# Optimization experiments

Hardware: AMD Instinct MI355X
Metric: run time of the kernel (lower is better)

Reference implementation:

```python
import jax, jax.numpy as jnp
import numpy as np

D = 512       # hidden_size (attention defaults hardcode 512)
N = 8         # num_heads
H = D // N    # depth per head = 64
FF = 2048     # FFN filter size (hardcoded)
EPS = 1e-6


def _layer_norm(x, gamma, beta):
    # matches functional layer_norm: biased variance, eps inside sqrt
    mean = jnp.mean(x, axis=-1, keepdims=True)
    var = jnp.mean((x - mean) ** 2, axis=-1, keepdims=True)
    return gamma * ((x - mean) / jnp.sqrt(var + EPS)) + beta


def setup_inputs() -> dict:
    key = jax.random.key(0)
    ks = jax.random.split(key, 12)
    B, S = 8, 1024
    s = lambda k, shape, scale: jax.random.normal(k, shape, jnp.float32) * scale
    return {
        "inputs": s(ks[0], (B, S, D), 1.0),
        "attention_bias": jnp.zeros((B, 1, 1, S), jnp.float32),
        "ln1_g": jnp.ones((D,), jnp.float32),
        "ln1_b": jnp.zeros((D,), jnp.float32),
        "wq": s(ks[1], (D, N, H), D ** -0.5),
        "wk": s(ks[2], (D, N, H), D ** -0.5),
        "wv": s(ks[3], (D, N, H), D ** -0.5),
        "wo": s(ks[4], (N, H, D), D ** -0.5),
        "ln2_g": jnp.ones((D,), jnp.float32),
        "ln2_b": jnp.zeros((D,), jnp.float32),
        "w1": s(ks[5], (D, FF), D ** -0.5),
        "b1": jnp.zeros((FF,), jnp.float32),
        "w2": s(ks[6], (FF, D), FF ** -0.5),
        "b2": jnp.zeros((D,), jnp.float32),
    }


def reference(inputs, attention_bias, ln1_g, ln1_b, wq, wk, wv, wo,
              ln2_g, ln2_b, w1, b1, w2, b2):
    # --- self-attention block (pre-LN, residual) ---
    y = _layer_norm(inputs, ln1_g, ln1_b)
    q = jnp.einsum('bsd,dnh->bsnh', y, wq) * (H ** -0.5)
    k = jnp.einsum('bsd,dnh->bsnh', y, wk)
    v = jnp.einsum('bsd,dnh->bsnh', y, wv)
    # logits[b,n,f,t] = sum_h k[b,t,n,h] * q[b,f,n,h]
    logits = jnp.einsum('btnh,bfnh->bnft', k, q) + attention_bias
    weights = jax.nn.softmax(logits, axis=3)
    attn = jnp.einsum('bnft,btnh->bfnh', weights, v)
    attn_out = jnp.einsum('bfnh,nhd->bfd', attn, wo)
    x = inputs + attn_out

    # --- FFN block (pre-LN, residual) ---
    y2 = _layer_norm(x, ln2_g, ln2_b)
    h = jax.nn.relu(jnp.einsum('bsd,df->bsf', y2, w1) + b1)
    ffn_out = jnp.einsum('bsf,fd->bsd', h, w2) + b2
    return x + ffn_out
```

## Files before the change

### kernel.cpp

```cpp
#include <hip/hip_runtime.h>
#include <stdint.h>

typedef unsigned short u16;
typedef __attribute__((ext_vector_type(8))) __bf16 bf16x8;
typedef __attribute__((ext_vector_type(2))) __bf16 bf16x2;
typedef __attribute__((ext_vector_type(4))) float f32x4;

__device__ __forceinline__ float bf2f(u16 u) {
    union { unsigned int i; float f; } c; c.i = ((unsigned int)u) << 16; return c.f;
}
__device__ __forceinline__ u16 f2bf_sw(float f) {
    union { float f; unsigned int i; } c; c.f = f;
    unsigned int u = c.i;
    u += 0x7FFFu + ((u >> 16) & 1u);
    return (u16)(u >> 16);
}
__device__ __forceinline__ unsigned f2bf2(float lo, float hi) {
#if __has_builtin(__builtin_amdgcn_cvt_pk_bf16_f32)
    union { bf16x2 v; unsigned u; } c;
    c.v = __builtin_amdgcn_cvt_pk_bf16_f32(lo, hi);
    return c.u;
#else
    return (unsigned)f2bf_sw(lo) | ((unsigned)f2bf_sw(hi) << 16);
#endif
}
__device__ __forceinline__ u16 f2bf(float f) {
#if __has_builtin(__builtin_amdgcn_cvt_pk_bf16_f32)
    return (u16)(f2bf2(f, 0.f) & 0xFFFFu);
#else
    return f2bf_sw(f);
#endif
}
__device__ __forceinline__ bool sniff_f32(const unsigned* probe) {
    return probe && ((*probe & 0xFFFFu) == 0u);
}
__device__ __forceinline__ float lde(const void* p, size_t i, bool isf32) {
    return isf32 ? ((const float*)p)[i] : bf2f(((const u16*)p)[i]);
}
__device__ __forceinline__ void g2lds16(const void* g, void* l) {
    __builtin_amdgcn_global_load_lds(
        (__attribute__((address_space(1))) void*)(uintptr_t)g,
        (__attribute__((address_space(3))) void*)(unsigned int)(uintptr_t)l,
        16, 0, 0);
}
__device__ __forceinline__ void fence_bar() {
    __builtin_amdgcn_sched_barrier(0);
    __builtin_amdgcn_s_barrier();
    __builtin_amdgcn_sched_barrier(0);
}

__global__ void prep_weights(const void* __restrict__ wq, const void* __restrict__ wk,
                             const void* __restrict__ wv, const void* __restrict__ wo,
                             const void* __restrict__ w1, const void* __restrict__ w2,
                             u16* __restrict__ wqkvT, u16* __restrict__ woT,
                             u16* __restrict__ w1T, u16* __restrict__ w2T,
                             const unsigned* probe) {
    __shared__ u16 t[32][33];
    const bool isf32 = sniff_f32(probe);
    const int id = blockIdx.x;
    const void* src; u16* dst; int R, C, cb, rb; float scale = 1.f;
    if (id < 1024) {
        const int which = id >> 8, tl = id & 255;
        R = 512; C = 512; cb = (tl & 15) * 32; rb = (tl >> 4) * 32;
        if (which == 0)      { src = wq; dst = wqkvT;              scale = 0.18033688011112042f; }
        else if (which == 1) { src = wk; dst = wqkvT + 512 * 512; }
        else if (which == 2) { src = wv; dst = wqkvT + 1024 * 512; }
        else                 { src = wo; dst = woT; }
    } else if (id < 2048) {
        const int tl = id - 1024; src = w1; dst = w1T; R = 512; C = 2048;
        cb = (tl & 63) * 32; rb = (tl >> 6) * 32;
    } else {
        const int tl = id - 2048; src = w2; dst = w2T; R = 2048; C = 512;
        cb = (tl & 15) * 32; rb = (tl >> 4) * 32;
    }
    const int tx = threadIdx.x, ty = threadIdx.y;
#pragma unroll
    for (int i = 0; i < 4; i++)
        t[ty + i * 8][tx] = f2bf(lde(src, (size_t)(rb + ty + i * 8) * C + cb + tx, isf32));
    __syncthreads();
#pragma unroll
    for (int i = 0; i < 4; i++) {
        float v = bf2f(t[tx][ty + i * 8]) * scale;
        dst[(size_t)(cb + ty + i * 8) * R + rb + tx] = f2bf(v);
    }
}

__global__ __launch_bounds__(256) void ln_any(const void* __restrict__ x,
                                              const void* __restrict__ gw,
                                              const void* __restrict__ bw,
                                              u16* __restrict__ y,
                                              const unsigned* probe_x,
                                              const unsigned* probe_gb) {
    const bool xf32 = sniff_f32(probe_x);
    const bool gf32 = sniff_f32(probe_gb);
    const int lane = threadIdx.x & 63, wave = threadIdx.x >> 6;
    const int r = blockIdx.x * 4 + wave;
    union U8 { uint4 v; u16 s[8]; };
    float xs[8];
    if (xf32) {
        const float4* xr = (const float4*)((const float*)x + (size_t)r * 512 + lane * 8);
        float4 p0 = xr[0], p1 = xr[1];
        xs[0]=p0.x; xs[1]=p0.y; xs[2]=p0.z; xs[3]=p0.w;
        xs[4]=p1.x; xs[5]=p1.y; xs[6]=p1.z; xs[7]=p1.w;
    } else {
        U8 xu; xu.v = *(const uint4*)((const u16*)x + (size_t)r * 512 + lane * 8);
#pragma unroll
        for (int j = 0; j < 8; j++) xs[j] = bf2f(xu.s[j]);
    }
    float s1 = 0.f, s2 = 0.f;
#pragma unroll
    for (int j = 0; j < 8; j++) { s1 += xs[j]; s2 += xs[j] * xs[j]; }
#pragma unroll
    for (int d = 1; d < 64; d <<= 1) { s1 += __shfl_xor(s1, d); s2 += __shfl_xor(s2, d); }
    const float mean = s1 * (1.f / 512.f);
    const float var = s2 * (1.f / 512.f) - mean * mean;
    const float rstd = rsqrtf(var + 1e-6f);
    float gs[8], bs[8];
    if (gf32) {
        const float4* gr = (const float4*)((const float*)gw + lane * 8);
        const float4* br = (const float4*)((const float*)bw + lane * 8);
        float4 g0 = gr[0], g1 = gr[1], b0 = br[0], b1 = br[1];
        gs[0]=g0.x; gs[1]=g0.y; gs[2]=g0.z; gs[3]=g0.w; gs[4]=g1.x; gs[5]=g1.y; gs[6]=g1.z; gs[7]=g1.w;
        bs[0]=b0.x; bs[1]=b0.y; bs[2]=b0.z; bs[3]=b0.w; bs[4]=b1.x; bs[5]=b1.y; bs[6]=b1.z; bs[7]=b1.w;
    } else {
        U8 gu; gu.v = *(const uint4*)((const u16*)gw + lane * 8);
        U8 bu; bu.v = *(const uint4*)((const u16*)bw + lane * 8);
#pragma unroll
        for (int j = 0; j < 8; j++) { gs[j] = bf2f(gu.s[j]); bs[j] = bf2f(bu.s[j]); }
    }
    uint4 ov;
    float o[8];
#pragma unroll
    for (int j = 0; j < 8; j++) o[j] = gs[j] * ((xs[j] - mean) * rstd) + bs[j];
    ov.x = f2bf2(o[0], o[1]); ov.y = f2bf2(o[2], o[3]);
    ov.z = f2bf2(o[4], o[5]); ov.w = f2bf2(o[6], o[7]);
    *(uint4*)(y + (size_t)r * 512 + lane * 8) = ov;
}

template <int EPI, int TM>
__global__ __launch_bounds__(256, 2) void gemm_bt(const u16* __restrict__ A,
                                                  const u16* __restrict__ Bt,
                                                  const void* __restrict__ bias,
                                                  const void* __restrict__ res,
                                                  void* __restrict__ out,
                                                  u16* __restrict__ out2,
                                                  const unsigned* probe,
                                                  int M, int N, int K) {
    constexpr int ACH = TM / 16;
    constexpr int MI = TM / 32;
    __shared__ __align__(16) u16 lA[2][TM * 32];
    __shared__ __align__(16) u16 lB[2][128 * 32];
    const int tid = threadIdx.x, wave = tid >> 6, lane = tid & 63;
    const int m0 = blockIdx.x * TM, n0 = blockIdx.y * 128;
    const int wm = (wave >> 1) * (TM / 2), wn = (wave & 1) * 64;
    const int row = lane & 15, quad = lane >> 4;
    f32x4 acc[MI][4];
#pragma unroll
    for (int i = 0; i < MI; i++)
#pragma unroll
        for (int j = 0; j < 4; j++) acc[i][j] = (f32x4){0.f, 0.f, 0.f, 0.f};
    const u16* Ab = A + (size_t)m0 * K;
    const u16* Bb = Bt + (size_t)n0 * K;

    auto stage = [&](int buf, int k0) {
#pragma unroll
        for (int c = 0; c < (ACH + 8 + 3) / 4; c++) {
            const int ch = c * 4 + wave;
            if (ch < ACH) {
                const int e = ch * 64 + lane;
                const int r = e >> 2, col = (e & 3) * 8;
                g2lds16(Ab + (size_t)r * K + k0 + col, (char*)lA[buf] + ch * 1024);
            } else if (ch < ACH + 8) {
                const int c2 = ch - ACH;
                const int e = c2 * 64 + lane;
                const int r = e >> 2, col = (e & 3) * 8;
                g2lds16(Bb + (size_t)r * K + k0 + col, (char*)lB[buf] + c2 * 1024);
            }
        }
    };

    stage(0, 0);
    int cur = 0;
    for (int k0 = 0; k0 < K; k0 += 32) {
        __syncthreads();
        if (k0 + 32 < K) stage(cur ^ 1, k0 + 32);
        bf16x8 af[MI], bfr[4];
#pragma unroll
        for (int t = 0; t < MI; t++)
            af[t]  = *(const bf16x8*)(lA[cur] + (wm + t * 16 + row) * 32 + quad * 8);
#pragma unroll
        for (int t = 0; t < 4; t++)
            bfr[t] = *(const bf16x8*)(lB[cur] + (wn + t * 16 + row) * 32 + quad * 8);
#pragma unroll
        for (int i = 0; i < MI; i++)
#pragma unroll
            for (int j = 0; j < 4; j++)
                acc[i][j] = __builtin_amdgcn_mfma_f32_16x16x32_bf16(af[i], bfr[j], acc[i][j], 0, 0, 0);
        cur ^= 1;
    }
    const bool isf32 = sniff_f32(probe);
#pragma unroll
    for (int i = 0; i < MI; i++) {
        const int gm = m0 + wm + i * 16 + quad * 4;
#pragma unroll
        for (int j = 0; j < 4; j++) {
            const int gn = n0 + wn + j * 16 + row;
            float bv = 0.f;
            if (EPI == 2 || EPI == 3) bv = lde(bias, gn, isf32);
#pragma unroll
            for (int r = 0; r < 4; r++) {
                float v = acc[i][j][r];
                const int gmr = gm + r;
                size_t idx = (size_t)gmr * N + gn;
                if (EPI == 1) {
                    ((u16*)out)[idx] = f2bf(v + lde(res, idx, isf32));
                } else if (EPI == 2) {
                    v += bv;
                    ((u16*)out)[idx] = f2bf(v > 0.f ? v : 0.f);
                } else if (EPI == 3) {
                    v += bv + bf2f(((const u16*)res)[idx]);
                    if (isf32) ((float*)out)[idx] = v;
                    else       ((u16*)out)[idx] = f2bf(v);
                } else {
                    if (gn < 1024) {
                        ((u16*)out)[(size_t)gmr * 1024 + gn] = f2bf(v);
                    } else {
                        const int j2 = gn - 1024, n = j2 >> 6, h2 = j2 & 63;
                        const int b = gmr >> 10, t = gmr & 1023;
                        const int ut = t & 31, vt = ut & 15;
                        const int tP = (t & ~31) | ((vt >> 2) * 8 + ((ut >> 4) << 2) + (vt & 3));
                        out2[(((size_t)b * 8 + n) * 64 + h2) * 1024 + tP] = f2bf(v);
                    }
                }
            }
        }
    }
}

__global__ __launch_bounds__(512, 8) void attn_fused(const u16* __restrict__ qk,
                                                     const u16* __restrict__ vT,
                                                     const void* __restrict__ biasp,
                                                     u16* __restrict__ attn,
                                                     const unsigned* probe) {
    __shared__ __align__(16) char smem[36864];
    u16* lKb = (u16*)smem;
    u16* lVb = (u16*)(smem + 16384);
    char* lB = smem + 32768;
    const bool isf32 = sniff_f32(probe);
    const int tid = threadIdx.x, wave = tid >> 6, lane = tid & 63;
    const int wid = wave & 3, grp = wave >> 2;
    const int row = lane & 15, quad = lane >> 4;
    const int g0 = (quad ^ (row & 7)) * 8;
    const int gV = (quad ^ (row & 3)) * 8;
    const int bn = blockIdx.x, b = bn >> 3, n = bn & 7;
    const int f0 = blockIdx.y * 64;
    const u16* Qg = qk + (size_t)(b * 1024 + f0) * 1024 + n * 64;
    const u16* Kg = qk + (size_t)(b * 1024) * 1024 + 512 + n * 64;
    const u16* Vg = vT + (size_t)bn * 65536;

    auto stageKV = [&](int slot, int t0) {
        const int rk = wid * 8 + (lane >> 3);
        const int ck = ((lane & 7) ^ (rk & 7)) * 8;
        g2lds16(Kg + (size_t)(t0 + rk) * 1024 + ck, (char*)(lKb + slot * 2048) + wid * 1024);
        const int rv = wid * 16 + (lane >> 2);
        const int cv = ((lane & 3) ^ (rv & 3)) * 8;
        g2lds16(Vg + (size_t)rv * 1024 + t0 + cv, (char*)(lVb + slot * 2048) + wid * 1024);
    };

    bf16x8 bq[2];
    {
        const u16* qrow = Qg + (size_t)(wid * 16 + row) * 1024;
        bq[0] = *(const bf16x8*)(qrow + quad * 8);
        bq[1] = *(const bf16x8*)(qrow + (4 + quad) * 8);
    }
    if (grp == 0) {
        if (isf32)
            g2lds16((const float*)biasp + (size_t)b * 1024 + wid * 256 + lane * 4, lB + wid * 1024);
        else if (wid < 2)
            g2lds16((const u16*)biasp + (size_t)b * 1024 + wid * 512 + lane * 8, lB + wid * 1024);
    }
    stageKV(grp * 2,     grp * 32);
    stageKV(grp * 2 + 1, (2 + grp) * 32);
    asm volatile("s_waitcnt vmcnt(0)" ::: "memory");
    fence_bar();

    float l_i = 0.f;
    f32x4 oacc[4];
#pragma unroll
    for (int h = 0; h < 4; h++) oacc[h] = (f32x4){0.f, 0.f, 0.f, 0.f};

    auto compute = [&](int slot, int t0) {
        const u16* lKc = lKb + slot * 2048;
        const u16* lVc = lVb + slot * 2048;
        f32x4 s2[2];
        s2[0] = (f32x4){0.f, 0.f, 0.f, 0.f};
        s2[1] = (f32x4){0.f, 0.f, 0.f, 0.f};
#pragma unroll
        for (int nt = 0; nt < 2; nt++) {
            const int tr = nt * 16 + row;
            bf16x8 ak0 = *(const bf16x8*)(lKc + tr * 64 + g0);
            s2[nt] = __builtin_amdgcn_mfma_f32_16x16x32_bf16(ak0, bq[0], s2[nt], 0, 0, 0);
            bf16x8 ak1 = *(const bf16x8*)(lKc + tr * 64 + (g0 ^ 32));
            s2[nt] = __builtin_amdgcn_mfma_f32_16x16x32_bf16(ak1, bq[1], s2[nt], 0, 0, 0);
        }
#pragma unroll
        for (int nt = 0; nt < 2; nt++) {
            const int tl = t0 + nt * 16 + quad * 4;
            float bv4[4];
            if (isf32) {
                float4 t4 = *(const float4*)((const float*)lB + tl);
                bv4[0] = t4.x; bv4[1] = t4.y; bv4[2] = t4.z; bv4[3] = t4.w;
            } else {
                union { uint2 v; u16 s[4]; } bu;
                bu.v = *(const uint2*)((const u16*)lB + tl);
#pragma unroll
                for (int r = 0; r < 4; r++) bv4[r] = bf2f(bu.s[r]);
            }
#pragma unroll
            for (int r = 0; r < 4; r++) {
                float p = __builtin_exp2f(fmaf(bv4[r], 1.4426950408889634f, s2[nt][r]));
                s2[nt][r] = p;
                l_i += p;
            }
        }
        union { unsigned u[4]; bf16x8 v8; } bb;
        bb.u[0] = f2bf2(s2[0][0], s2[0][1]);
        bb.u[1] = f2bf2(s2[0][2], s2[0][3]);
        bb.u[2] = f2bf2(s2[1][0], s2[1][1]);
        bb.u[3] = f2bf2(s2[1][2], s2[1][3]);
#pragma unroll
        for (int ht = 0; ht < 4; ht++) {
            bf16x8 av = *(const bf16x8*)(lVc + (ht * 16 + row) * 32 + gV);
            oacc[ht] = __builtin_amdgcn_mfma_f32_16x16x32_bf16(av, bb.v8, oacc[ht], 0, 0, 0);
        }
    };

#pragma unroll 1
    for (int s = 0; s < 15; s++) {
        compute(grp * 2 + (s & 1), (2 * s + grp) * 32);
        fence_bar();
        if (s <= 13) {
            stageKV(grp * 2 + (s & 1), (2 * (s + 2) + grp) * 32);
            asm volatile("s_waitcnt vmcnt(2)" ::: "memory");
        } else {
            asm volatile("s_waitcnt vmcnt(0)" ::: "memory");
        }
        fence_bar();
    }
    compute(grp * 2 + 1, (30 + grp) * 32);

    __syncthreads();
    float* scr = (float*)smem;
    float* scrL = scr + 4608;
    if (grp == 1) {
#pragma unroll
        for (int ht = 0; ht < 4; ht++)
            *(f32x4*)(scr + wid * 1152 + (ht * 64 + lane) * 4) = oacc[ht];
        scrL[wid * 64 + lane] = l_i;
    }
    __syncthreads();
    if (grp == 0) {
#pragma unroll
        for (int ht = 0; ht < 4; ht++)
            oacc[ht] += *(const f32x4*)(scr + wid * 1152 + (ht * 64 + lane) * 4);
        l_i += scrL[wid * 64 + lane];
        l_i += __shfl_xor(l_i, 16);
        l_i += __shfl_xor(l_i, 32);
        const float inv = 1.f / l_i;
        const int f = f0 + wid * 16 + row;
#pragma unroll
        for (int ht = 0; ht < 4; ht++) {
            uint2 ov;
            ov.x = f2bf2(oacc[ht][0] * inv, oacc[ht][1] * inv);
            ov.y = f2bf2(oacc[ht][2] * inv, oacc[ht][3] * inv);
            *(uint2*)(attn + (size_t)(b * 1024 + f) * 512 + n * 64 + ht * 16 + quad * 4) = ov;
        }
    }
}

extern "C" void kernel_launch(void* const* d_in, const int* in_sizes, int n_in,
                              void* d_out, int out_size, void* d_ws, size_t ws_size,
                              hipStream_t stream) {
    const void* inp  = d_in[0];
    const void* ab   = d_in[1];
    const void* ln1g = d_in[2];
    const void* ln1b = d_in[3];
    const void* wq   = d_in[4];
    const void* wk   = d_in[5];
    const void* wv   = d_in[6];
    const void* wo   = d_in[7];
    const void* ln2g = d_in[8];
    const void* ln2b = d_in[9];
    const void* w1   = d_in[10];
    const void* b1   = d_in[11];
    const void* w2   = d_in[12];
    const void* b2   = d_in[13];
    const unsigned* probe = (const unsigned*)d_in[2];

    char* ws = (char*)d_ws;
    size_t off = 0;
    auto alloc = [&](size_t bytes) -> void* { void* p = ws + off; off += bytes; return p; };
    u16* wqkvT = (u16*)alloc(1536 * 512 * 2);
    u16* woT   = (u16*)alloc(512 * 512 * 2);
    u16* w1T   = (u16*)alloc(2048 * 512 * 2);
    u16* w2T   = (u16*)alloc(512 * 2048 * 2);
    u16* ybuf  = (u16*)alloc((size_t)8192 * 512 * 2);
    u16* qk    = (u16*)alloc((size_t)8192 * 1024 * 2);
    u16* vT    = (u16*)alloc((size_t)64 * 64 * 1024 * 2);
    u16* attn  = (u16*)alloc((size_t)8192 * 512 * 2);
    u16* xbf   = (u16*)alloc((size_t)8192 * 512 * 2);
    u16* hbuf  = qk;

    prep_weights<<<3072, dim3(32, 8), 0, stream>>>(wq, wk, wv, wo, w1, w2,
                                                   wqkvT, woT, w1T, w2T, probe);
    ln_any<<<2048, 256, 0, stream>>>(inp, ln1g, ln1b, ybuf, probe, probe);
    gemm_bt<4, 128><<<dim3(64, 12), 256, 0, stream>>>(ybuf, wqkvT, nullptr, nullptr, qk, vT, nullptr, 8192, 1536, 512);
    attn_fused<<<dim3(64, 16), 512, 0, stream>>>(qk, vT, ab, attn, probe);
    gemm_bt<1, 64><<<dim3(128, 4), 256, 0, stream>>>(attn, woT, nullptr, inp, xbf, nullptr, probe, 8192, 512, 512);
    ln_any<<<2048, 256, 0, stream>>>(xbf, ln2g, ln2b, ybuf, nullptr, probe);
    gemm_bt<2, 128><<<dim3(64, 16), 256, 0, stream>>>(ybuf, w1T, b1, nullptr, hbuf, nullptr, probe, 8192, 2048, 512);
    gemm_bt<3, 64><<<dim3(128, 4), 256, 0, stream>>>(hbuf, w2T, b2, xbf, (u16*)d_out, nullptr, probe, 8192, 512, 2048);
}
```

Measured before the change: 251.2 us.

## Fuse weight prep with LN1 and fuse Wo projection with residual and LN2

Merges the weight transpose kernel and the first layer norm into one launch using block-index ranges. Replaces the Wo GEMM plus the separate LN2 kernel with a new full-row GEMM (16 rows by 512 cols per block) that adds the residual, computes row mean and variance through shuffles and LDS partials, and writes both x and the normalized y. This removes two launches and an extra read of x. In exchange the new GEMM uses small M tiles, so each block re-streams the full Wo matrix and gets less reuse per block.

```diff
diff --git a/kernel.cpp b/kernel.cpp
--- a/kernel.cpp
+++ b/kernel.cpp
@@ -49,92 +49,88 @@
     __builtin_amdgcn_sched_barrier(0);
 }
 
-__global__ void prep_weights(const void* __restrict__ wq, const void* __restrict__ wk,
-                             const void* __restrict__ wv, const void* __restrict__ wo,
-                             const void* __restrict__ w1, const void* __restrict__ w2,
-                             u16* __restrict__ wqkvT, u16* __restrict__ woT,
-                             u16* __restrict__ w1T, u16* __restrict__ w2T,
-                             const unsigned* probe) {
+__global__ __launch_bounds__(256) void prep_ln(const void* __restrict__ wq, const void* __restrict__ wk,
+                                               const void* __restrict__ wv, const void* __restrict__ wo,
+                                               const void* __restrict__ w1, const void* __restrict__ w2,
+                                               u16* __restrict__ wqkvT, u16* __restrict__ woT,
+                                               u16* __restrict__ w1T, u16* __restrict__ w2T,
+                                               const void* __restrict__ inp, const void* __restrict__ ln1g,
+                                               const void* __restrict__ ln1b, u16* __restrict__ ybuf,
+                                               const unsigned* probe) {
     __shared__ u16 t[32][33];
     const bool isf32 = sniff_f32(probe);
     const int id = blockIdx.x;
-    const void* src; u16* dst; int R, C, cb, rb; float scale = 1.f;
-    if (id < 1024) {
-        const int which = id >> 8, tl = id & 255;
-        R = 512; C = 512; cb = (tl & 15) * 32; rb = (tl >> 4) * 32;
-        if (which == 0)      { src = wq; dst = wqkvT;              scale = 0.18033688011112042f; }
-        else if (which == 1) { src = wk; dst = wqkvT + 512 * 512; }
-        else if (which == 2) { src = wv; dst = wqkvT + 1024 * 512; }
-        else                 { src = wo; dst = woT; }
-    } else if (id < 2048) {
-        const int tl = id - 1024; src = w1; dst = w1T; R = 512; C = 2048;
-        cb = (tl & 63) * 32; rb = (tl >> 6) * 32;
+    const int tid = threadIdx.x;
+    if (id < 3072) {
+        const void* src; u16* dst; int R, C, cb, rb; float scale = 1.f;
+        if (id < 1024) {
+            const int which = id >> 8, tl = id & 255;
+            R = 512; C = 512; cb = (tl & 15) * 32; rb = (tl >> 4) * 32;
+            if (which == 0)      { src = wq; dst = wqkvT;              scale = 0.18033688011112042f; }
+            else if (which == 1) { src = wk; dst = wqkvT + 512 * 512; }
+            else if (which == 2) { src = wv; dst = wqkvT + 1024 * 512; }
+            else                 { src = wo; dst = woT; }
+        } else if (id < 2048) {
+            const int tl = id - 1024; src = w1; dst = w1T; R = 512; C = 2048;
+            cb = (tl & 63) * 32; rb = (tl >> 6) * 32;
+        } else {
+            const int tl = id - 2048; src = w2; dst = w2T; R = 2048; C = 512;
+            cb = (tl & 15) * 32; rb = (tl >> 4) * 32;
+        }
+        const int tx = tid & 31, ty = tid >> 5;
+#pragma unroll
+        for (int i = 0; i < 4; i++)
+            t[ty + i * 8][tx] = f2bf(lde(src, (size_t)(rb + ty + i * 8) * C + cb + tx, isf32));
+        __syncthreads();
+#pragma unroll
+        for (int i = 0; i < 4; i++) {
+            float v = bf2f(t[tx][ty + i * 8]) * scale;
+            dst[(size_t)(cb + ty + i * 8) * R + rb + tx] = f2bf(v);
+        }
     } else {
-        const int tl = id - 2048; src = w2; dst = w2T; R = 2048; C = 512;
-        cb = (tl & 15) * 32; rb = (tl >> 4) * 32;
-    }
-    const int tx = threadIdx.x, ty = threadIdx.y;
-#pragma unroll
-    for (int i = 0; i < 4; i++)
-        t[ty + i * 8][tx] = f2bf(lde(src, (size_t)(rb + ty + i * 8) * C + cb + tx, isf32));
-    __syncthreads();
-#pragma unroll
-    for (int i = 0; i < 4; i++) {
-        float v = bf2f(t[tx][ty + i * 8]) * scale;
-        dst[(size_t)(cb + ty + i * 8) * R + rb + tx] = f2bf(v);
-    }
-}
-
-__global__ __launch_bounds__(256) void ln_any(const void* __restrict__ x,
-                                              const void* __restrict__ gw,
-                                              const void* __restrict__ bw,
-                                              u16* __restrict__ y,
-                                              const unsigned* probe_x,
-                                              const unsigned* probe_gb) {
-    const bool xf32 = sniff_f32(probe_x);
-    const bool gf32 = sniff_f32(probe_gb);
-    const int lane = threadIdx.x & 63, wave = threadIdx.x >> 6;
-    const int r = blockIdx.x * 4 + wave;
-    union U8 { uint4 v; u16 s[8]; };
-    float xs[8];
-    if (xf32) {
-        const float4* xr = (const float4*)((const float*)x + (size_t)r * 512 + lane * 8);
-        float4 p0 = xr[0], p1 = xr[1];
-        xs[0]=p0.x; xs[1]=p0.y; xs[2]=p0.z; xs[3]=p0.w;
-        xs[4]=p1.x; xs[5]=p1.y; xs[6]=p1.z; xs[7]=p1.w;
-    } else {
-        U8 xu; xu.v = *(const uint4*)((const u16*)x + (size_t)r * 512 + lane * 8);
-#pragma unroll
-        for (int j = 0; j < 8; j++) xs[j] = bf2f(xu.s[j]);
-    }
-    float s1 = 0.f, s2 = 0.f;
-#pragma unroll
-    for (int j = 0; j < 8; j++) { s1 += xs[j]; s2 += xs[j] * xs[j]; }
-#pragma unroll
-    for (int d = 1; d < 64; d <<= 1) { s1 += __shfl_xor(s1, d); s2 += __shfl_xor(s2, d); }
-    const float mean = s1 * (1.f / 512.f);
-    const float var = s2 * (1.f / 512.f) - mean * mean;
-    const float rstd = rsqrtf(var + 1e-6f);
-    float gs[8], bs[8];
-    if (gf32) {
-        const float4* gr = (const float4*)((const float*)gw + lane * 8);
-        const float4* br = (const float4*)((const float*)bw + lane * 8);
-        float4 g0 = gr[0], g1 = gr[1], b0 = br[0], b1 = br[1];
-        gs[0]=g0.x; gs[1]=g0.y; gs[2]=g0.z; gs[3]=g0.w; gs[4]=g1.x; gs[5]=g1.y; gs[6]=g1.z; gs[7]=g1.w;
-        bs[0]=b0.x; bs[1]=b0.y; bs[2]=b0.z; bs[3]=b0.w; bs[4]=b1.x; bs[5]=b1.y; bs[6]=b1.z; bs[7]=b1.w;
-    } else {
-        U8 gu; gu.v = *(const uint4*)((const u16*)gw + lane * 8);
-        U8 bu; bu.v = *(const uint4*)((const u16*)bw + lane * 8);
-#pragma unroll
-        for (int j = 0; j < 8; j++) { gs[j] = bf2f(gu.s[j]); bs[j] = bf2f(bu.s[j]); }
-    }
-    uint4 ov;
-    float o[8];
-#pragma unroll
-    for (int j = 0; j < 8; j++) o[j] = gs[j] * ((xs[j] - mean) * rstd) + bs[j];
-    ov.x = f2bf2(o[0], o[1]); ov.y = f2bf2(o[2], o[3]);
-    ov.z = f2bf2(o[4], o[5]); ov.w = f2bf2(o[6], o[7]);
-    *(uint4*)(y + (size_t)r * 512 + lane * 8) = ov;
+        const int lane = tid & 63, wave = tid >> 6;
+        const int r = (id - 3072) * 4 + wave;
+        union U8 { uint4 v; u16 s[8]; };
+        float xs[8];
+        if (isf32) {
+            const float4* xr = (const float4*)((const float*)inp + (size_t)r * 512 + lane * 8);
+            float4 p0 = xr[0], p1 = xr[1];
+            xs[0]=p0.x; xs[1]=p0.y; xs[2]=p0.z; xs[3]=p0.w;
+            xs[4]=p1.x; xs[5]=p1.y; xs[6]=p1.z; xs[7]=p1.w;
+        } else {
+            U8 xu; xu.v = *(const uint4*)((const u16*)inp + (size_t)r * 512 + lane * 8);
+#pragma unroll
+            for (int j = 0; j < 8; j++) xs[j] = bf2f(xu.s[j]);
+        }
+        float s1 = 0.f, s2 = 0.f;
+#pragma unroll
+        for (int j = 0; j < 8; j++) { s1 += xs[j]; s2 += xs[j] * xs[j]; }
+#pragma unroll
+        for (int d = 1; d < 64; d <<= 1) { s1 += __shfl_xor(s1, d); s2 += __shfl_xor(s2, d); }
+        const float mean = s1 * (1.f / 512.f);
+        const float var = s2 * (1.f / 512.f) - mean * mean;
+        const float rstd = rsqrtf(var + 1e-6f);
+        float gs[8], bs[8];
+        if (isf32) {
+            const float4* gr = (const float4*)((const float*)ln1g + lane * 8);
+            const float4* br = (const float4*)((const float*)ln1b + lane * 8);
+            float4 g0 = gr[0], g1 = gr[1], b0 = br[0], b1 = br[1];
+            gs[0]=g0.x; gs[1]=g0.y; gs[2]=g0.z; gs[3]=g0.w; gs[4]=g1.x; gs[5]=g1.y; gs[6]=g1.z; gs[7]=g1.w;
+            bs[0]=b0.x; bs[1]=b0.y; bs[2]=b0.z; bs[3]=b0.w; bs[4]=b1.x; bs[5]=b1.y; bs[6]=b1.z; bs[7]=b1.w;
+        } else {
+            U8 gu; gu.v = *(const uint4*)((const u16*)ln1g + lane * 8);
+            U8 bu; bu.v = *(const uint4*)((const u16*)ln1b + lane * 8);
+#pragma unroll
+            for (int j = 0; j < 8; j++) { gs[j] = bf2f(gu.s[j]); bs[j] = bf2f(bu.s[j]); }
+        }
+        uint4 ov;
+        float o[8];
+#pragma unroll
+        for (int j = 0; j < 8; j++) o[j] = gs[j] * ((xs[j] - mean) * rstd) + bs[j];
+        ov.x = f2bf2(o[0], o[1]); ov.y = f2bf2(o[2], o[3]);
+        ov.z = f2bf2(o[4], o[5]); ov.w = f2bf2(o[6], o[7]);
+        *(uint4*)(ybuf + (size_t)r * 512 + lane * 8) = ov;
+    }
 }
 
 template <int EPI, int TM>
@@ -212,9 +208,7 @@
                 float v = acc[i][j][r];
                 const int gmr = gm + r;
                 size_t idx = (size_t)gmr * N + gn;
-                if (EPI == 1) {
-                    ((u16*)out)[idx] = f2bf(v + lde(res, idx, isf32));
-                } else if (EPI == 2) {
+                if (EPI == 2) {
                     v += bv;
                     ((u16*)out)[idx] = f2bf(v > 0.f ? v : 0.f);
                 } else if (EPI == 3) {
@@ -233,6 +227,118 @@
                     }
                 }
             }
+        }
+    }
+}
+
+__global__ __launch_bounds__(256, 2) void gemm_wo_ln(const u16* __restrict__ A,
+                                                     const u16* __restrict__ Bt,
+                                                     const void* __restrict__ res,
+                                                     const void* __restrict__ gw,
+                                                     const void* __restrict__ bw,
+                                                     u16* __restrict__ ybuf,
+                                                     u16* __restrict__ xbf,
+                                                     const unsigned* probe) {
+    __shared__ __align__(16) u16 lA[2][16 * 32];
+    __shared__ __align__(16) u16 lB[2][512 * 32];
+    const int tid = threadIdx.x, wave = tid >> 6, lane = tid & 63;
+    const int row = lane & 15, quad = lane >> 4;
+    const int m0 = blockIdx.x * 16;
+    const int wn = wave * 128;
+    f32x4 acc[8];
+#pragma unroll
+    for (int j = 0; j < 8; j++) acc[j] = (f32x4){0.f, 0.f, 0.f, 0.f};
+    const u16* Ab = A + (size_t)m0 * 512;
+
+    auto stage = [&](int buf, int k0) {
+#pragma unroll
+        for (int c = 0; c < 9; c++) {
+            const int ch = c * 4 + wave;
+            if (ch < 1) {
+                const int r = lane >> 2, col = (lane & 3) * 8;
+                g2lds16(Ab + (size_t)r * 512 + k0 + col, (char*)lA[buf]);
+            } else if (ch < 33) {
+                const int c2 = ch - 1;
+                const int e = c2 * 64 + lane;
+                const int r = e >> 2, col = (e & 3) * 8;
+                g2lds16(Bt + (size_t)r * 512 + k0 + col, (char*)lB[buf] + c2 * 1024);
+            }
+        }
+    };
+
+    stage(0, 0);
+    int cur = 0;
+    for (int k0 = 0; k0 < 512; k0 += 32) {
+        __syncthreads();
+        if (k0 + 32 < 512) stage(cur ^ 1, k0 + 32);
+        bf16x8 af = *(const bf16x8*)(lA[cur] + row * 32 + quad * 8);
+        bf16x8 bfr[8];
+#pragma unroll
+        for (int j = 0; j < 8; j++)
+            bfr[j] = *(const bf16x8*)(lB[cur] + (wn + j * 16 + row) * 32 + quad * 8);
+#pragma unroll
+        for (int j = 0; j < 8; j++)
+            acc[j] = __builtin_amdgcn_mfma_f32_16x16x32_bf16(af, bfr[j], acc[j], 0, 0, 0);
+        cur ^= 1;
+    }
+
+    const bool isf32 = sniff_f32(probe);
+    float x[8][4];
+    float s1[4] = {0.f, 0.f, 0.f, 0.f}, s2[4] = {0.f, 0.f, 0.f, 0.f};
+#pragma unroll
+    for (int j = 0; j < 8; j++) {
+        const int gn = wn + j * 16 + row;
+#pragma unroll
+        for (int rr = 0; rr < 4; rr++) {
+            const int gm = m0 + quad * 4 + rr;
+            float v = acc[j][rr] + lde(res, (size_t)gm * 512 + gn, isf32);
+            x[j][rr] = v;
+            s1[rr] += v; s2[rr] += v * v;
+        }
+    }
+#pragma unroll
+    for (int rr = 0; rr < 4; rr++)
+#pragma unroll
+        for (int d = 1; d < 16; d <<= 1) {
+            s1[rr] += __shfl_xor(s1[rr], d);
+            s2[rr] += __shfl_xor(s2[rr], d);
+        }
+    __syncthreads();
+    float* part = (float*)lA;
+    if (row == 0) {
+#pragma unroll
+        for (int rr = 0; rr < 4; rr++) {
+            part[(wave * 16 + quad * 4 + rr) * 2 + 0] = s1[rr];
+            part[(wave * 16 + quad * 4 + rr) * 2 + 1] = s2[rr];
+        }
+    }
+    __syncthreads();
+    float mean[4], rstd[4];
+#pragma unroll
+    for (int rr = 0; rr < 4; rr++) {
+        const int r16 = quad * 4 + rr;
+        float a = part[(r16) * 2] + part[(16 + r16) * 2] + part[(32 + r16) * 2] + part[(48 + r16) * 2];
+        float q = part[(r16) * 2 + 1] + part[(16 + r16) * 2 + 1] + part[(32 + r16) * 2 + 1] + part[(48 + r16) * 2 + 1];
+        mean[rr] = a * (1.f / 512.f);
+        float var = q * (1.f / 512.f) - mean[rr] * mean[rr];
+        rstd[rr] = rsqrtf(var + 1e-6f);
+    }
+    float gs[8], bs[8];
+#pragma unroll
+    for (int j = 0; j < 8; j++) {
+        const int gn = wn + j * 16 + row;
+        gs[j] = lde(gw, gn, isf32);
+        bs[j] = lde(bw, gn, isf32);
+    }
+#pragma unroll
+    for (int j = 0; j < 8; j++) {
+        const int gn = wn + j * 16 + row;
+#pragma unroll
+        for (int rr = 0; rr < 4; rr++) {
+            const int gm = m0 + quad * 4 + rr;
+            const size_t idx = (size_t)gm * 512 + gn;
+            xbf[idx]  = f2bf(x[j][rr]);
+            ybuf[idx] = f2bf(gs[j] * ((x[j][rr] - mean[rr]) * rstd[rr]) + bs[j]);
         }
     }
 }
@@ -411,13 +517,12 @@
     u16* xbf   = (u16*)alloc((size_t)8192 * 512 * 2);
     u16* hbuf  = qk;
 
-    prep_weights<<<3072, dim3(32, 8), 0, stream>>>(wq, wk, wv, wo, w1, w2,
-                                                   wqkvT, woT, w1T, w2T, probe);
-    ln_any<<<2048, 256, 0, stream>>>(inp, ln1g, ln1b, ybuf, probe, probe);
+    prep_ln<<<5120, 256, 0, stream>>>(wq, wk, wv, wo, w1, w2,
+                                      wqkvT, woT, w1T, w2T,
+                                      inp, ln1g, ln1b, ybuf, probe);
     gemm_bt<4, 128><<<dim3(64, 12), 256, 0, stream>>>(ybuf, wqkvT, nullptr, nullptr, qk, vT, nullptr, 8192, 1536, 512);
     attn_fused<<<dim3(64, 16), 512, 0, stream>>>(qk, vT, ab, attn, probe);
-    gemm_bt<1, 64><<<dim3(128, 4), 256, 0, stream>>>(attn, woT, nullptr, inp, xbf, nullptr, probe, 8192, 512, 512);
-    ln_any<<<2048, 256, 0, stream>>>(xbf, ln2g, ln2b, ybuf, nullptr, probe);
+    gemm_wo_ln<<<512, 256, 0, stream>>>(attn, woT, inp, ln2g, ln2b, ybuf, xbf, probe);
     gemm_bt<2, 128><<<dim3(64, 16), 256, 0, stream>>>(ybuf, w1T, b1, nullptr, hbuf, nullptr, probe, 8192, 2048, 512);
     gemm_bt<3, 64><<<dim3(128, 4), 256, 0, stream>>>(hbuf, w2T, b2, xbf, (u16*)d_out, nullptr, probe, 8192, 512, 2048);
 }
```

Result: no change. 249.6 us (-0.6%).
